# Kernel optimization log

Measured on AMD Instinct MI355X. Metric: run time of the kernel, lower is better.

The kernel has to match this reference:

```python
import jax, jax.numpy as jnp
import numpy as np

NUM_HEADS = 8
NUM_POINTS = 4


def _bilinear(img, xs, ys):
    """Bilinear sample with zero padding (grid_sample align_corners=False).
    img: [N, H, W, C]; xs, ys: [N, P] pixel-space coords. Returns [N, P, C]."""
    H, W = img.shape[1], img.shape[2]
    x0 = jnp.floor(xs)
    y0 = jnp.floor(ys)
    wx = xs - x0
    wy = ys - y0
    x0i = x0.astype(jnp.int32)
    y0i = y0.astype(jnp.int32)

    def g(ix, iy):
        valid = ((ix >= 0) & (ix < W) & (iy >= 0) & (iy < H)).astype(img.dtype)
        ixc = jnp.clip(ix, 0, W - 1)
        iyc = jnp.clip(iy, 0, H - 1)
        v = jax.vmap(lambda im, yy, xx: im[yy, xx])(img, iyc, ixc)  # [N,P,C]
        return v * valid[..., None]

    return (g(x0i, y0i) * ((1 - wx) * (1 - wy))[..., None]
            + g(x0i + 1, y0i) * (wx * (1 - wy))[..., None]
            + g(x0i, y0i + 1) * ((1 - wx) * wy)[..., None]
            + g(x0i + 1, y0i + 1) * (wx * wy)[..., None])


def setup_inputs() -> dict:
    key = jax.random.key(0)
    ks = jax.random.split(key, 10)
    BN, C, H, W = 12, 256, 40, 100
    nq = H * W
    hp = NUM_HEADS * NUM_POINTS
    s = 1.0 / np.sqrt(C).astype(np.float32)
    return {
        "img_feats": jax.random.normal(ks[0], (BN, C, H, W), jnp.float32),
        "warp_grid": jax.random.uniform(ks[1], (BN, H, W, 2), jnp.float32),
        "reference_points": jax.random.uniform(ks[2], (BN, nq, 1, 2), jnp.float32),
        "Wv": jax.random.normal(ks[3], (C, C), jnp.float32) * s,
        "bv": jnp.zeros((C,), jnp.float32),
        "Woff": jax.random.normal(ks[4], (C, hp * 2), jnp.float32) * 0.01,
        "boff": jax.random.normal(ks[5], (hp * 2,), jnp.float32) * 0.5,
        "Wattn": jax.random.normal(ks[6], (C, hp), jnp.float32) * 0.01,
        "battn": jnp.zeros((hp,), jnp.float32),
        "Wout": jax.random.normal(ks[7], (C, C), jnp.float32) * s,
        "bout": jnp.zeros((C,), jnp.float32),
    }


def reference(img_feats, warp_grid, reference_points,
              Wv, bv, Woff, boff, Wattn, battn, Wout, bout):
    BN, C, H, W = img_feats.shape
    heads, pts = NUM_HEADS, NUM_POINTS
    hd = C // heads
    nq = H * W

    feat = img_feats.transpose(0, 2, 3, 1)  # [BN, H, W, C]

    # BEVWarp: bilinear warp of image features at the projected grid ([0,1] normed)
    gx = warp_grid[..., 0].reshape(BN, -1) * W - 0.5
    gy = warp_grid[..., 1].reshape(BN, -1) * H - 0.5
    warped = _bilinear(feat, gx, gy)          # [BN, nq, C] -> value
    query = feat.reshape(BN, nq, C)           # flattened img feats -> query

    # MultiScaleDeformableAttention, num_levels=1
    v = (warped @ Wv + bv).reshape(BN, nq, heads, hd)
    off = (query @ Woff + boff).reshape(BN, nq, heads, pts, 2)
    attn = jax.nn.softmax((query @ Wattn + battn).reshape(BN, nq, heads, pts), axis=-1)

    norm = jnp.array([W, H], dtype=img_feats.dtype)
    loc = reference_points.reshape(BN, nq, 1, 1, 2) + off / norm  # [BN,nq,h,p,2]

    vh = v.transpose(0, 2, 1, 3).reshape(BN * heads, H, W, hd)
    lx = (loc[..., 0] * W - 0.5).transpose(0, 2, 1, 3).reshape(BN * heads, nq * pts)
    ly = (loc[..., 1] * H - 0.5).transpose(0, 2, 1, 3).reshape(BN * heads, nq * pts)
    sampled = _bilinear(vh, lx, ly).reshape(BN, heads, nq, pts, hd)

    agg = jnp.einsum('bhqpd,bqhp->bqhd', sampled, attn).reshape(BN, nq, C)
    out = agg @ Wout + bout + query  # output_proj + residual (dropout=0 at eval)
    return out.transpose(0, 2, 1).reshape(BN, C, H, W)
```

## Files before the change

### kernel.cpp

```cpp
#include <hip/hip_runtime.h>

#define DEVINL __device__ __forceinline__

typedef __attribute__((ext_vector_type(4))) float f32x4;
typedef __attribute__((ext_vector_type(8))) short short8;

constexpr int kBN = 12, kC = 256, kH = 40, kW = 100;
constexpr int kNQ = kH * kW;
constexpr int kM = kBN * kNQ;

DEVINL float bflo(uint p) { union { uint i; float f; } v; v.i = p << 16; return v.f; }
DEVINL float bfhi(uint p) { union { uint i; float f; } v; v.i = p & 0xffff0000u; return v.f; }
DEVINL ushort f2bf(float f) {
  union { float f; uint i; } v; v.f = f;
  uint i = v.i;
  return (ushort)((i + 0x7fffu + ((i >> 16) & 1u)) >> 16);
}
DEVINL uint pack2(float a, float b) { return (uint)f2bf(a) | ((uint)f2bf(b) << 16); }

DEVINL void mfma_bf16(f32x4& acc, short8 a, short8 b) {
  acc = __builtin_amdgcn_mfma_f32_16x16x32_bf16(a, b, acc, 0, 0, 0);
}

DEVINL void gload16(const ushort* g, char* lds) {
  __builtin_amdgcn_global_load_lds(
      (const __attribute__((address_space(1))) uint*)g,
      (__attribute__((address_space(3))) uint*)lds, 16, 0, 0);
}

DEVINL void acc8(float* acc, uint4 d, float wv) {
  acc[0] += wv * bflo(d.x); acc[1] += wv * bfhi(d.x);
  acc[2] += wv * bflo(d.y); acc[3] += wv * bfhi(d.y);
  acc[4] += wv * bflo(d.z); acc[5] += wv * bfhi(d.z);
  acc[6] += wv * bflo(d.w); acc[7] += wv * bfhi(d.w);
}

__global__ __launch_bounds__(256) void k_wt_all(const float* __restrict__ Wv,
                                                const float* __restrict__ Woff,
                                                const float* __restrict__ Wattn,
                                                const float* __restrict__ Wout,
                                                ushort* __restrict__ WvT,
                                                ushort* __restrict__ WoffT,
                                                ushort* __restrict__ WattnT,
                                                ushort* __restrict__ WoutT) {
  int idx = blockIdx.x * 256 + threadIdx.x;
  const float* W; ushort* WT; int N, base;
  if (idx < 65536)       { W = Wv;    WT = WvT;    N = 256; base = 0; }
  else if (idx < 81920)  { W = Woff;  WT = WoffT;  N = 64;  base = 65536; }
  else if (idx < 90112)  { W = Wattn; WT = WattnT; N = 32;  base = 81920; }
  else if (idx < 155648) { W = Wout;  WT = WoutT;  N = 256; base = 90112; }
  else return;
  int i = idx - base;
  int n = i >> 8, k = i & 255;
  WT[i] = f2bf(W[k * N + n]);
}

__global__ __launch_bounds__(256) void k_transpose(const float* __restrict__ img,
                                                   ushort* __restrict__ feat) {
  __shared__ ushort tile[64][66];
  int b = blockIdx.z, c0 = blockIdx.y * 64, q0 = blockIdx.x * 64;
  int t = threadIdx.x;
  int ql = t & 63, cl = t >> 6;
#pragma unroll
  for (int i = 0; i < 16; ++i) {
    int c = cl + i * 4, q = q0 + ql;
    float v = (q < kNQ) ? img[(size_t)(b * kC + c0 + c) * kNQ + q] : 0.f;
    tile[c][ql] = f2bf(v);
  }
  __syncthreads();
#pragma unroll
  for (int i = 0; i < 2; ++i) {
    int idx = t + i * 256;
    int qlo = idx >> 3, cg = idx & 7;
    int q = q0 + qlo;
    if (q < kNQ) {
      ushort tmp[8];
#pragma unroll
      for (int j = 0; j < 8; ++j) tmp[j] = tile[cg * 8 + j][qlo];
      *(uint4*)(feat + ((size_t)b * kNQ + q) * kC + c0 + cg * 8) = *(uint4*)tmp;
    }
  }
}

__global__ __launch_bounds__(256) void k_warp(const ushort* __restrict__ feat,
                                              const float* __restrict__ grid,
                                              ushort* __restrict__ warped) {
  int orig = blockIdx.x;
  int n = (orig & 7) * 750 + (orig >> 3);
  int t = threadIdx.x;
  int ql = t >> 5, g = t & 31;
  int gq = n * 8 + ql;
  int b = gq / kNQ;
  float gx = grid[(size_t)gq * 2 + 0] * kW - 0.5f;
  float gy = grid[(size_t)gq * 2 + 1] * kH - 0.5f;
  float x0f = floorf(gx), y0f = floorf(gy);
  int x0 = (int)x0f, y0 = (int)y0f;
  float wx = gx - x0f, wy = gy - y0f;
  float acc[8];
#pragma unroll
  for (int i = 0; i < 8; ++i) acc[i] = 0.f;
  const ushort* fb = feat + (size_t)b * kNQ * kC + g * 8;
#pragma unroll
  for (int ty = 0; ty < 2; ++ty) {
    int iy = y0 + ty;
    if (iy < 0 || iy >= kH) continue;
    float wyv = ty ? wy : 1.f - wy;
#pragma unroll
    for (int tx = 0; tx < 2; ++tx) {
      int ix = x0 + tx;
      if (ix < 0 || ix >= kW) continue;
      float wv = wyv * (tx ? wx : 1.f - wx);
      uint4 d = *(const uint4*)(fb + (size_t)(iy * kW + ix) * kC);
      acc8(acc, d, wv);
    }
  }
  uint o[4] = {pack2(acc[0], acc[1]), pack2(acc[2], acc[3]),
               pack2(acc[4], acc[5]), pack2(acc[6], acc[7])};
  *(uint4*)(warped + (size_t)gq * kC + g * 8) = *(uint4*)o;
}

template <int EPI>
__global__ __launch_bounds__(256) void k_gemm256(const ushort* __restrict__ A,
                                                 const ushort* __restrict__ BT,
                                                 const float* __restrict__ bias,
                                                 ushort* __restrict__ Obf,
                                                 float* __restrict__ Ofp,
                                                 const float* __restrict__ resid) {
  extern __shared__ char smem[];
  const int t = threadIdx.x, wave = t >> 6, lane = t & 63;
  const int l15 = lane & 15, l4 = lane >> 4;
  const int b = blockIdx.x / 63, mb = blockIdx.x % 63;
  const int q0 = mb * 64;
  const int nrows = (kNQ - q0 < 64) ? (kNQ - q0) : 64;
  const int n0w = wave * 64;
  const int ra = t >> 2, ca = t & 3;
  const int rac = (ra < nrows) ? ra : (nrows - 1);
  const int sca = ca ^ ((ra >> 1) & 3);
  const ushort* gA = A + ((size_t)b * kNQ + q0 + rac) * 256 + sca * 8;
  const ushort* gB = BT + (size_t)ra * 256 + sca * 8;

  f32x4 acc[4][4];
#pragma unroll
  for (int i = 0; i < 4; ++i)
#pragma unroll
    for (int j = 0; j < 4; ++j) acc[i][j] = (f32x4)0.f;

  auto STAGE = [&](int buf, int kk) {
    char* Asb = smem + buf * 20480;
    char* Bsb = Asb + 4096;
    gload16(gA + kk, Asb + t * 16);
#pragma unroll
    for (int i = 0; i < 4; ++i)
      gload16(gB + (size_t)i * 64 * 256 + kk, Bsb + (i * 256 + t) * 16);
  };

  STAGE(0, 0);
  int cur = 0;
#pragma unroll 1
  for (int step = 0; step < 8; ++step) {
    if (step < 7) {
      STAGE(cur ^ 1, (step + 1) * 32);
      asm volatile("s_waitcnt vmcnt(5)" ::: "memory");
    } else {
      asm volatile("s_waitcnt vmcnt(0)" ::: "memory");
    }
    __builtin_amdgcn_s_barrier();
    asm volatile("" ::: "memory");
    char* Asb = smem + cur * 20480;
    char* Bsb = Asb + 4096;
    short8 af[4], bf[4];
#pragma unroll
    for (int mf = 0; mf < 4; ++mf) {
      int r = mf * 16 + l15;
      int sl = l4 ^ ((r >> 1) & 3);
      af[mf] = *(const short8*)(Asb + r * 64 + sl * 16);
    }
#pragma unroll
    for (int nf = 0; nf < 4; ++nf) {
      int r = n0w + nf * 16 + l15;
      int sl = l4 ^ ((r >> 1) & 3);
      bf[nf] = *(const short8*)(Bsb + r * 64 + sl * 16);
    }
#pragma unroll
    for (int mf = 0; mf < 4; ++mf)
#pragma unroll
      for (int nf = 0; nf < 4; ++nf) mfma_bf16(acc[mf][nf], af[mf], bf[nf]);
    asm volatile("" ::: "memory");
    __builtin_amdgcn_s_barrier();
    cur ^= 1;
  }

  if (EPI == 0) {
#pragma unroll
    for (int mf = 0; mf < 4; ++mf) {
      if (mf * 16 >= nrows) continue;
      int q = q0 + mf * 16 + l4 * 4;
#pragma unroll
      for (int nf = 0; nf < 4; ++nf) {
        int col = n0w + nf * 16 + l15;
        float bv = bias[col];
        int h = col >> 5, ch = col & 31;
        ushort* dst = Obf + (size_t)(b * 8 + h) * kNQ * 32 + ch;
#pragma unroll
        for (int j = 0; j < 4; ++j)
          dst[(size_t)(q + j) * 32] = f2bf(acc[mf][nf][j] + bv);
      }
    }
  } else {
    float* Tw = (float*)(smem + wave * 4352);
#pragma unroll
    for (int nf = 0; nf < 4; ++nf) {
      float bv = bias[n0w + nf * 16 + l15];
#pragma unroll
      for (int mf = 0; mf < 4; ++mf)
#pragma unroll
        for (int j = 0; j < 4; ++j)
          Tw[l15 * 68 + mf * 16 + l4 * 4 + j] = acc[mf][nf][j] + bv;
      int c = l15, rs = l4 * 16;
      if (rs < nrows) {
        int col = n0w + nf * 16 + c;
        size_t gi = ((size_t)b * kC + col) * kNQ + q0 + rs;
#pragma unroll
        for (int k = 0; k < 4; ++k) {
          float4 tv = *(float4*)(&Tw[c * 68 + rs + k * 4]);
          float4 rv = *(const float4*)(resid + gi + k * 4);
          tv.x += rv.x; tv.y += rv.y; tv.z += rv.z; tv.w += rv.w;
          *(float4*)(Ofp + gi + k * 4) = tv;
        }
      }
    }
  }
}

__global__ __launch_bounds__(256) void k_offattn(const ushort* __restrict__ A,
                                                 const ushort* __restrict__ WoffT,
                                                 const ushort* __restrict__ WattnT,
                                                 const float* __restrict__ boff,
                                                 const float* __restrict__ battn,
                                                 const float* __restrict__ refp,
                                                 float* __restrict__ samp) {
  extern __shared__ char smem[];
  float* T = (float*)smem;
  const int t = threadIdx.x, wave = t >> 6, lane = t & 63;
  const int l15 = lane & 15, l4 = lane >> 4;
  const int b = blockIdx.x / 63, mb = blockIdx.x % 63;
  const int q0 = mb * 64;
  const int nrows = (kNQ - q0 < 64) ? (kNQ - q0) : 64;
  const int wr = wave >> 1, wc = wave & 1;
  const int ra = t >> 2, ca = t & 3;
  const int rac = (ra < nrows) ? ra : (nrows - 1);
  const int sca = ca ^ ((ra >> 1) & 3);
  const ushort* gA  = A + ((size_t)b * kNQ + q0 + rac) * 256 + sca * 8;
  const ushort* gB0 = WoffT + (size_t)ra * 256 + sca * 8;
  const ushort* gB1 = WattnT + (size_t)ra * 256 + sca * 8;

  f32x4 acc[2][3];
#pragma unroll
  for (int i = 0; i < 2; ++i)
#pragma unroll
    for (int j = 0; j < 3; ++j) acc[i][j] = (f32x4)0.f;

  auto STAGE = [&](int buf, int kk) {
    char* Asb = smem + buf * 10240;
    char* Bsb = Asb + 4096;
    gload16(gA + kk, Asb + t * 16);
    gload16(gB0 + kk, Bsb + t * 16);
    if (t < 128) gload16(gB1 + kk, Bsb + (256 + t) * 16);
  };

  STAGE(0, 0);
  int cur = 0;
#pragma unroll 1
  for (int step = 0; step < 8; ++step) {
    if (step < 7) {
      STAGE(cur ^ 1, (step + 1) * 32);
      if (wave < 2) asm volatile("s_waitcnt vmcnt(3)" ::: "memory");
      else          asm volatile("s_waitcnt vmcnt(2)" ::: "memory");
    } else {
      asm volatile("s_waitcnt vmcnt(0)" ::: "memory");
    }
    __builtin_amdgcn_s_barrier();
    asm volatile("" ::: "memory");
    char* Asb = smem + cur * 10240;
    char* Bsb = Asb + 4096;
    short8 af[2], bf[3];
#pragma unroll
    for (int mf = 0; mf < 2; ++mf) {
      int r = wr * 32 + mf * 16 + l15;
      int sl = l4 ^ ((r >> 1) & 3);
      af[mf] = *(const short8*)(Asb + r * 64 + sl * 16);
    }
#pragma unroll
    for (int nf = 0; nf < 3; ++nf) {
      int r = wc * 48 + nf * 16 + l15;
      int sl = l4 ^ ((r >> 1) & 3);
      bf[nf] = *(const short8*)(Bsb + r * 64 + sl * 16);
    }
#pragma unroll
    for (int mf = 0; mf < 2; ++mf)
#pragma unroll
      for (int nf = 0; nf < 3; ++nf) mfma_bf16(acc[mf][nf], af[mf], bf[nf]);
    asm volatile("" ::: "memory");
    __builtin_amdgcn_s_barrier();
    cur ^= 1;
  }

#pragma unroll
  for (int nf = 0; nf < 3; ++nf) {
    int col = wc * 48 + nf * 16 + l15;
    float bv = (col < 64) ? boff[col] : battn[col - 64];
#pragma unroll
    for (int mf = 0; mf < 2; ++mf)
#pragma unroll
      for (int j = 0; j < 4; ++j) {
        int row = wr * 32 + mf * 16 + l4 * 4 + j;
        T[row * 101 + col] = acc[mf][nf][j] + bv;
      }
  }
  __syncthreads();
  int row = t >> 2;
  if (row < nrows) {
    int q = q0 + row;
    float refx = refp[((size_t)b * kNQ + q) * 2 + 0] * kW - 0.5f;
    float refy = refp[((size_t)b * kNQ + q) * 2 + 1] * kH - 0.5f;
#pragma unroll
    for (int hi2 = 0; hi2 < 2; ++hi2) {
      int h = (t & 3) + hi2 * 4;
      float sx[4], sy[4], lg[4];
#pragma unroll
      for (int p = 0; p < 4; ++p) {
        sx[p] = refx + T[row * 101 + h * 8 + p * 2 + 0];
        sy[p] = refy + T[row * 101 + h * 8 + p * 2 + 1];
        lg[p] = T[row * 101 + 64 + h * 4 + p];
      }
      float mx = fmaxf(fmaxf(lg[0], lg[1]), fmaxf(lg[2], lg[3]));
      float e[4], s = 0.f;
#pragma unroll
      for (int p = 0; p < 4; ++p) { e[p] = __expf(lg[p] - mx); s += e[p]; }
      float inv = 1.f / s;
      float* dst = samp + (((size_t)(b * 8 + h) * kNQ + q) * 4) * 3;
#pragma unroll
      for (int p = 0; p < 4; ++p) {
        dst[p * 3 + 0] = sx[p];
        dst[p * 3 + 1] = sy[p];
        dst[p * 3 + 2] = e[p] * inv;
      }
    }
  }
}

__global__ __launch_bounds__(256) void k_sample(const ushort* __restrict__ v,
                                                const float* __restrict__ samp,
                                                ushort* __restrict__ agg) {
  int orig = blockIdx.x;
  int n = (orig & 7) * 756 + (orig >> 3);
  int plane = n / 63, chunk = n - plane * 63;
  int t = threadIdx.x;
  int ql = t >> 2, g = t & 3;
  int q = chunk * 64 + ql;
  if (q >= kNQ) return;
  int b = plane >> 3, h = plane & 7;
  const ushort* pv = v + (size_t)plane * kNQ * 32 + g * 8;
  const int lane = t & 63, gbase = lane & ~3;

  const float* sp = samp + (((size_t)plane * kNQ + q) * 4 + g) * 3;
  float myx = sp[0], myy = sp[1], myw = sp[2];
  float acc[8];
#pragma unroll
  for (int i = 0; i < 8; ++i) acc[i] = 0.f;
#pragma unroll
  for (int p = 0; p < 4; ++p) {
    float sxp = __shfl(myx, gbase + p);
    float syp = __shfl(myy, gbase + p);
    float wp  = __shfl(myw, gbase + p);
    float x0f = floorf(sxp), y0f = floorf(syp);
    int x0 = (int)x0f, y0 = (int)y0f;
    float wx = sxp - x0f, wy = syp - y0f;
#pragma unroll
    for (int ty = 0; ty < 2; ++ty) {
      int iy = y0 + ty;
      if (iy < 0 || iy >= kH) continue;
      float wyv = ty ? wy : 1.f - wy;
#pragma unroll
      for (int tx = 0; tx < 2; ++tx) {
        int ix = x0 + tx;
        if (ix < 0 || ix >= kW) continue;
        float wv = wp * wyv * (tx ? wx : 1.f - wx);
        uint4 d = *(const uint4*)(pv + (size_t)(iy * kW + ix) * 32);
        acc8(acc, d, wv);
      }
    }
  }
  uint o[4] = {pack2(acc[0], acc[1]), pack2(acc[2], acc[3]),
               pack2(acc[4], acc[5]), pack2(acc[6], acc[7])};
  *(uint4*)(agg + ((size_t)b * kNQ + q) * kC + h * 32 + g * 8) = *(uint4*)o;
}

extern "C" void kernel_launch(void* const* d_in, const int* in_sizes, int n_in,
                              void* d_out, int out_size, void* d_ws, size_t ws_size,
                              hipStream_t stream) {
  const float* img   = (const float*)d_in[0];
  const float* grid  = (const float*)d_in[1];
  const float* refp  = (const float*)d_in[2];
  const float* Wv    = (const float*)d_in[3];
  const float* bv    = (const float*)d_in[4];
  const float* Woff  = (const float*)d_in[5];
  const float* boff  = (const float*)d_in[6];
  const float* Wattn = (const float*)d_in[7];
  const float* battn = (const float*)d_in[8];
  const float* Wout  = (const float*)d_in[9];
  const float* bout  = (const float*)d_in[10];
  float* out = (float*)d_out;

  char* ws = (char*)d_ws;
  const size_t SZ = (size_t)kM * kC * 2;
  ushort* feat   = (ushort*)(ws);
  ushort* warped = (ushort*)(ws + SZ);
  ushort* vbuf   = (ushort*)(ws + 2 * SZ);
  float*  samp   = (float*)(ws + 3 * SZ);
  ushort* WvT    = (ushort*)(ws + 4 * SZ);
  ushort* WoffT  = (ushort*)(ws + 4 * SZ + 131072);
  ushort* WattnT = (ushort*)(ws + 4 * SZ + 131072 + 32768);
  ushort* WoutT  = (ushort*)(ws + 4 * SZ + 131072 + 32768 + 16384);
  ushort* aggb   = warped;

  k_wt_all<<<608, 256, 0, stream>>>(Wv, Woff, Wattn, Wout, WvT, WoffT, WattnT, WoutT);
  k_transpose<<<dim3(63, 4, 12), 256, 0, stream>>>(img, feat);
  k_warp<<<6000, 256, 0, stream>>>(feat, grid, warped);
  k_gemm256<0><<<756, 256, 40960, stream>>>(warped, WvT, bv, vbuf, nullptr, nullptr);
  k_offattn<<<756, 256, 25856, stream>>>(feat, WoffT, WattnT, boff, battn, refp, samp);
  k_sample<<<6048, 256, 0, stream>>>(vbuf, samp, aggb);
  k_gemm256<1><<<756, 256, 40960, stream>>>(aggb, WoutT, bout, nullptr, out, img);
}
```

Before: 122.6 us.

## Merge prep and warp/offattn kernels, retile GEMMs to 128-row blocks, read bf16 residual

Fuses the weight-transpose and image-transpose launches into one kernel, and merges the bilinear warp with the offset/attention GEMM into one launch split by block index. It also replaces the 64-row GEMM with a 128-row, 512-thread tile that covers all 256 columns, and makes the output epilogue read the residual from the bf16 transposed features instead of the fp32 image. The aim is to cut launch overhead and tail effects and to improve weight reuse per block. The costs are a residual that is now rounded to bf16, strided 2-byte residual loads, and heavier blocks that may lower occupancy.

```diff
diff --git a/kernel.cpp b/kernel.cpp
--- a/kernel.cpp
+++ b/kernel.cpp
@@ -35,222 +35,114 @@
   acc[6] += wv * bflo(d.w); acc[7] += wv * bfhi(d.w);
 }
 
-__global__ __launch_bounds__(256) void k_wt_all(const float* __restrict__ Wv,
-                                                const float* __restrict__ Woff,
-                                                const float* __restrict__ Wattn,
-                                                const float* __restrict__ Wout,
-                                                ushort* __restrict__ WvT,
-                                                ushort* __restrict__ WoffT,
-                                                ushort* __restrict__ WattnT,
-                                                ushort* __restrict__ WoutT) {
-  int idx = blockIdx.x * 256 + threadIdx.x;
-  const float* W; ushort* WT; int N, base;
-  if (idx < 65536)       { W = Wv;    WT = WvT;    N = 256; base = 0; }
-  else if (idx < 81920)  { W = Woff;  WT = WoffT;  N = 64;  base = 65536; }
-  else if (idx < 90112)  { W = Wattn; WT = WattnT; N = 32;  base = 81920; }
-  else if (idx < 155648) { W = Wout;  WT = WoutT;  N = 256; base = 90112; }
-  else return;
-  int i = idx - base;
-  int n = i >> 8, k = i & 255;
-  WT[i] = f2bf(W[k * N + n]);
-}
-
-__global__ __launch_bounds__(256) void k_transpose(const float* __restrict__ img,
-                                                   ushort* __restrict__ feat) {
+__global__ __launch_bounds__(256) void k_prep(const float* __restrict__ img,
+                                              ushort* __restrict__ feat,
+                                              const float* __restrict__ Wv,
+                                              const float* __restrict__ Woff,
+                                              const float* __restrict__ Wattn,
+                                              const float* __restrict__ Wout,
+                                              ushort* __restrict__ WvT,
+                                              ushort* __restrict__ WoffT,
+                                              ushort* __restrict__ WattnT,
+                                              ushort* __restrict__ WoutT) {
   __shared__ ushort tile[64][66];
-  int b = blockIdx.z, c0 = blockIdx.y * 64, q0 = blockIdx.x * 64;
-  int t = threadIdx.x;
-  int ql = t & 63, cl = t >> 6;
-#pragma unroll
-  for (int i = 0; i < 16; ++i) {
-    int c = cl + i * 4, q = q0 + ql;
-    float v = (q < kNQ) ? img[(size_t)(b * kC + c0 + c) * kNQ + q] : 0.f;
-    tile[c][ql] = f2bf(v);
-  }
-  __syncthreads();
-#pragma unroll
-  for (int i = 0; i < 2; ++i) {
-    int idx = t + i * 256;
-    int qlo = idx >> 3, cg = idx & 7;
-    int q = q0 + qlo;
-    if (q < kNQ) {
-      ushort tmp[8];
-#pragma unroll
-      for (int j = 0; j < 8; ++j) tmp[j] = tile[cg * 8 + j][qlo];
-      *(uint4*)(feat + ((size_t)b * kNQ + q) * kC + c0 + cg * 8) = *(uint4*)tmp;
-    }
-  }
-}
-
-__global__ __launch_bounds__(256) void k_warp(const ushort* __restrict__ feat,
-                                              const float* __restrict__ grid,
-                                              ushort* __restrict__ warped) {
-  int orig = blockIdx.x;
-  int n = (orig & 7) * 750 + (orig >> 3);
-  int t = threadIdx.x;
-  int ql = t >> 5, g = t & 31;
-  int gq = n * 8 + ql;
-  int b = gq / kNQ;
-  float gx = grid[(size_t)gq * 2 + 0] * kW - 0.5f;
-  float gy = grid[(size_t)gq * 2 + 1] * kH - 0.5f;
-  float x0f = floorf(gx), y0f = floorf(gy);
-  int x0 = (int)x0f, y0 = (int)y0f;
-  float wx = gx - x0f, wy = gy - y0f;
-  float acc[8];
-#pragma unroll
-  for (int i = 0; i < 8; ++i) acc[i] = 0.f;
-  const ushort* fb = feat + (size_t)b * kNQ * kC + g * 8;
-#pragma unroll
-  for (int ty = 0; ty < 2; ++ty) {
-    int iy = y0 + ty;
-    if (iy < 0 || iy >= kH) continue;
-    float wyv = ty ? wy : 1.f - wy;
-#pragma unroll
-    for (int tx = 0; tx < 2; ++tx) {
-      int ix = x0 + tx;
-      if (ix < 0 || ix >= kW) continue;
-      float wv = wyv * (tx ? wx : 1.f - wx);
-      uint4 d = *(const uint4*)(fb + (size_t)(iy * kW + ix) * kC);
-      acc8(acc, d, wv);
-    }
-  }
-  uint o[4] = {pack2(acc[0], acc[1]), pack2(acc[2], acc[3]),
-               pack2(acc[4], acc[5]), pack2(acc[6], acc[7])};
-  *(uint4*)(warped + (size_t)gq * kC + g * 8) = *(uint4*)o;
-}
-
-template <int EPI>
-__global__ __launch_bounds__(256) void k_gemm256(const ushort* __restrict__ A,
-                                                 const ushort* __restrict__ BT,
-                                                 const float* __restrict__ bias,
-                                                 ushort* __restrict__ Obf,
-                                                 float* __restrict__ Ofp,
-                                                 const float* __restrict__ resid) {
+  int bx = blockIdx.x, t = threadIdx.x;
+  if (bx < 3024) {
+    int qb = bx % 63, cb = (bx / 63) & 3, b = bx / 252;
+    int c0 = cb * 64, q0 = qb * 64;
+    int ql = t & 63, cl = t >> 6;
+#pragma unroll
+    for (int i = 0; i < 16; ++i) {
+      int c = cl + i * 4, q = q0 + ql;
+      float v = (q < kNQ) ? img[(size_t)(b * kC + c0 + c) * kNQ + q] : 0.f;
+      tile[c][ql] = f2bf(v);
+    }
+    __syncthreads();
+#pragma unroll
+    for (int i = 0; i < 2; ++i) {
+      int idx = t + i * 256;
+      int qlo = idx >> 3, cg = idx & 7;
+      int q = q0 + qlo;
+      if (q < kNQ) {
+        ushort tmp[8];
+#pragma unroll
+        for (int j = 0; j < 8; ++j) tmp[j] = tile[cg * 8 + j][qlo];
+        *(uint4*)(feat + ((size_t)b * kNQ + q) * kC + c0 + cg * 8) = *(uint4*)tmp;
+      }
+    }
+  } else {
+    int idx = (bx - 3024) * 256 + t;
+    const float* W; ushort* WT; int N, base;
+    if (idx < 65536)       { W = Wv;    WT = WvT;    N = 256; base = 0; }
+    else if (idx < 81920)  { W = Woff;  WT = WoffT;  N = 64;  base = 65536; }
+    else if (idx < 90112)  { W = Wattn; WT = WattnT; N = 32;  base = 81920; }
+    else if (idx < 155648) { W = Wout;  WT = WoutT;  N = 256; base = 90112; }
+    else return;
+    int i = idx - base;
+    int n = i >> 8, k = i & 255;
+    WT[i] = f2bf(W[k * N + n]);
+  }
+}
+
+__global__ __launch_bounds__(256) void k_warp_offattn(const ushort* __restrict__ feat,
+                                                      const float* __restrict__ grid,
+                                                      ushort* __restrict__ warped,
+                                                      const ushort* __restrict__ WoffT,
+                                                      const ushort* __restrict__ WattnT,
+                                                      const float* __restrict__ boff,
+                                                      const float* __restrict__ battn,
+                                                      const float* __restrict__ refp,
+                                                      float* __restrict__ samp) {
   extern __shared__ char smem[];
-  const int t = threadIdx.x, wave = t >> 6, lane = t & 63;
+  const int t = threadIdx.x;
+  int bx = blockIdx.x;
+
+  if (bx >= 756) {
+    int orig = bx - 756;
+    int n = (orig & 7) * 750 + (orig >> 3);
+    int ql = t >> 5, g = t & 31;
+    int gq = n * 8 + ql;
+    int b = gq / kNQ;
+    float gx = grid[(size_t)gq * 2 + 0] * kW - 0.5f;
+    float gy = grid[(size_t)gq * 2 + 1] * kH - 0.5f;
+    float x0f = floorf(gx), y0f = floorf(gy);
+    int x0 = (int)x0f, y0 = (int)y0f;
+    float wx = gx - x0f, wy = gy - y0f;
+    float acc[8];
+#pragma unroll
+    for (int i = 0; i < 8; ++i) acc[i] = 0.f;
+    const ushort* fb = feat + (size_t)b * kNQ * kC + g * 8;
+#pragma unroll
+    for (int ty = 0; ty < 2; ++ty) {
+      int iy = y0 + ty;
+      if (iy < 0 || iy >= kH) continue;
+      float wyv = ty ? wy : 1.f - wy;
+#pragma unroll
+      for (int tx = 0; tx < 2; ++tx) {
+        int ix = x0 + tx;
+        if (ix < 0 || ix >= kW) continue;
+        float wv = wyv * (tx ? wx : 1.f - wx);
+        uint4 d = *(const uint4*)(fb + (size_t)(iy * kW + ix) * kC);
+        acc8(acc, d, wv);
+      }
+    }
+    uint o[4] = {pack2(acc[0], acc[1]), pack2(acc[2], acc[3]),
+                 pack2(acc[4], acc[5]), pack2(acc[6], acc[7])};
+    *(uint4*)(warped + (size_t)gq * kC + g * 8) = *(uint4*)o;
+    return;
+  }
+
+  float* T = (float*)smem;
+  const int wave = t >> 6, lane = t & 63;
   const int l15 = lane & 15, l4 = lane >> 4;
-  const int b = blockIdx.x / 63, mb = blockIdx.x % 63;
-  const int q0 = mb * 64;
-  const int nrows = (kNQ - q0 < 64) ? (kNQ - q0) : 64;
-  const int n0w = wave * 64;
-  const int ra = t >> 2, ca = t & 3;
-  const int rac = (ra < nrows) ? ra : (nrows - 1);
-  const int sca = ca ^ ((ra >> 1) & 3);
-  const ushort* gA = A + ((size_t)b * kNQ + q0 + rac) * 256 + sca * 8;
-  const ushort* gB = BT + (size_t)ra * 256 + sca * 8;
-
-  f32x4 acc[4][4];
-#pragma unroll
-  for (int i = 0; i < 4; ++i)
-#pragma unroll
-    for (int j = 0; j < 4; ++j) acc[i][j] = (f32x4)0.f;
-
-  auto STAGE = [&](int buf, int kk) {
-    char* Asb = smem + buf * 20480;
-    char* Bsb = Asb + 4096;
-    gload16(gA + kk, Asb + t * 16);
-#pragma unroll
-    for (int i = 0; i < 4; ++i)
-      gload16(gB + (size_t)i * 64 * 256 + kk, Bsb + (i * 256 + t) * 16);
-  };
-
-  STAGE(0, 0);
-  int cur = 0;
-#pragma unroll 1
-  for (int step = 0; step < 8; ++step) {
-    if (step < 7) {
-      STAGE(cur ^ 1, (step + 1) * 32);
-      asm volatile("s_waitcnt vmcnt(5)" ::: "memory");
-    } else {
-      asm volatile("s_waitcnt vmcnt(0)" ::: "memory");
-    }
-    __builtin_amdgcn_s_barrier();
-    asm volatile("" ::: "memory");
-    char* Asb = smem + cur * 20480;
-    char* Bsb = Asb + 4096;
-    short8 af[4], bf[4];
-#pragma unroll
-    for (int mf = 0; mf < 4; ++mf) {
-      int r = mf * 16 + l15;
-      int sl = l4 ^ ((r >> 1) & 3);
-      af[mf] = *(const short8*)(Asb + r * 64 + sl * 16);
-    }
-#pragma unroll
-    for (int nf = 0; nf < 4; ++nf) {
-      int r = n0w + nf * 16 + l15;
-      int sl = l4 ^ ((r >> 1) & 3);
-      bf[nf] = *(const short8*)(Bsb + r * 64 + sl * 16);
-    }
-#pragma unroll
-    for (int mf = 0; mf < 4; ++mf)
-#pragma unroll
-      for (int nf = 0; nf < 4; ++nf) mfma_bf16(acc[mf][nf], af[mf], bf[nf]);
-    asm volatile("" ::: "memory");
-    __builtin_amdgcn_s_barrier();
-    cur ^= 1;
-  }
-
-  if (EPI == 0) {
-#pragma unroll
-    for (int mf = 0; mf < 4; ++mf) {
-      if (mf * 16 >= nrows) continue;
-      int q = q0 + mf * 16 + l4 * 4;
-#pragma unroll
-      for (int nf = 0; nf < 4; ++nf) {
-        int col = n0w + nf * 16 + l15;
-        float bv = bias[col];
-        int h = col >> 5, ch = col & 31;
-        ushort* dst = Obf + (size_t)(b * 8 + h) * kNQ * 32 + ch;
-#pragma unroll
-        for (int j = 0; j < 4; ++j)
-          dst[(size_t)(q + j) * 32] = f2bf(acc[mf][nf][j] + bv);
-      }
-    }
-  } else {
-    float* Tw = (float*)(smem + wave * 4352);
-#pragma unroll
-    for (int nf = 0; nf < 4; ++nf) {
-      float bv = bias[n0w + nf * 16 + l15];
-#pragma unroll
-      for (int mf = 0; mf < 4; ++mf)
-#pragma unroll
-        for (int j = 0; j < 4; ++j)
-          Tw[l15 * 68 + mf * 16 + l4 * 4 + j] = acc[mf][nf][j] + bv;
-      int c = l15, rs = l4 * 16;
-      if (rs < nrows) {
-        int col = n0w + nf * 16 + c;
-        size_t gi = ((size_t)b * kC + col) * kNQ + q0 + rs;
-#pragma unroll
-        for (int k = 0; k < 4; ++k) {
-          float4 tv = *(float4*)(&Tw[c * 68 + rs + k * 4]);
-          float4 rv = *(const float4*)(resid + gi + k * 4);
-          tv.x += rv.x; tv.y += rv.y; tv.z += rv.z; tv.w += rv.w;
-          *(float4*)(Ofp + gi + k * 4) = tv;
-        }
-      }
-    }
-  }
-}
-
-__global__ __launch_bounds__(256) void k_offattn(const ushort* __restrict__ A,
-                                                 const ushort* __restrict__ WoffT,
-                                                 const ushort* __restrict__ WattnT,
-                                                 const float* __restrict__ boff,
-                                                 const float* __restrict__ battn,
-                                                 const float* __restrict__ refp,
-                                                 float* __restrict__ samp) {
-  extern __shared__ char smem[];
-  float* T = (float*)smem;
-  const int t = threadIdx.x, wave = t >> 6, lane = t & 63;
-  const int l15 = lane & 15, l4 = lane >> 4;
-  const int b = blockIdx.x / 63, mb = blockIdx.x % 63;
+  const int b = bx / 63, mb = bx % 63;
   const int q0 = mb * 64;
   const int nrows = (kNQ - q0 < 64) ? (kNQ - q0) : 64;
   const int wr = wave >> 1, wc = wave & 1;
   const int ra = t >> 2, ca = t & 3;
   const int rac = (ra < nrows) ? ra : (nrows - 1);
   const int sca = ca ^ ((ra >> 1) & 3);
-  const ushort* gA  = A + ((size_t)b * kNQ + q0 + rac) * 256 + sca * 8;
+  const ushort* gA  = feat + ((size_t)b * kNQ + q0 + rac) * 256 + sca * 8;
   const ushort* gB0 = WoffT + (size_t)ra * 256 + sca * 8;
   const ushort* gB1 = WattnT + (size_t)ra * 256 + sca * 8;
 
@@ -344,6 +236,124 @@
         dst[p * 3 + 0] = sx[p];
         dst[p * 3 + 1] = sy[p];
         dst[p * 3 + 2] = e[p] * inv;
+      }
+    }
+  }
+}
+
+template <int EPI>
+__global__ __launch_bounds__(512) void k_gemm128(const ushort* __restrict__ A,
+                                                 const ushort* __restrict__ BT,
+                                                 const float* __restrict__ bias,
+                                                 ushort* __restrict__ Obf,
+                                                 float* __restrict__ Ofp,
+                                                 const ushort* __restrict__ feat) {
+  extern __shared__ char smem[];
+  const int t = threadIdx.x, wave = t >> 6, lane = t & 63;
+  const int l15 = lane & 15, l4 = lane >> 4;
+  const int b = blockIdx.x >> 5, mb = blockIdx.x & 31;
+  const int q0 = mb * 128;
+  const int nrows = (kNQ - q0 < 128) ? (kNQ - q0) : 128;
+  const int wr = wave >> 2, wc = wave & 3;
+  const int ra = t >> 2, ca = t & 3;
+  const int rac = (ra < nrows) ? ra : (nrows - 1);
+  const int sca = ca ^ ((ra >> 1) & 3);
+  const ushort* gA = A + ((size_t)b * kNQ + q0 + rac) * 256 + sca * 8;
+  const ushort* gB = BT + (size_t)ra * 256 + sca * 8;
+
+  f32x4 acc[4][4];
+#pragma unroll
+  for (int i = 0; i < 4; ++i)
+#pragma unroll
+    for (int j = 0; j < 4; ++j) acc[i][j] = (f32x4)0.f;
+
+  auto STAGE = [&](int buf, int kk) {
+    char* Asb = smem + buf * 24576;
+    char* Bsb = Asb + 8192;
+    gload16(gA + kk, Asb + t * 16);
+#pragma unroll
+    for (int i = 0; i < 2; ++i)
+      gload16(gB + (size_t)i * 128 * 256 + kk, Bsb + (i * 512 + t) * 16);
+  };
+
+  STAGE(0, 0);
+  int cur = 0;
+#pragma unroll 1
+  for (int step = 0; step < 8; ++step) {
+    if (step < 7) {
+      STAGE(cur ^ 1, (step + 1) * 32);
+      asm volatile("s_waitcnt vmcnt(3)" ::: "memory");
+    } else {
+      asm volatile("s_waitcnt vmcnt(0)" ::: "memory");
+    }
+    __builtin_amdgcn_s_barrier();
+    asm volatile("" ::: "memory");
+    char* Asb = smem + cur * 24576;
+    char* Bsb = Asb + 8192;
+    short8 af[4], bf[4];
+#pragma unroll
+    for (int mf = 0; mf < 4; ++mf) {
+      int r = wr * 64 + mf * 16 + l15;
+      int sl = l4 ^ ((r >> 1) & 3);
+      af[mf] = *(const short8*)(Asb + r * 64 + sl * 16);
+    }
+#pragma unroll
+    for (int nf = 0; nf < 4; ++nf) {
+      int r = wc * 64 + nf * 16 + l15;
+      int sl = l4 ^ ((r >> 1) & 3);
+      bf[nf] = *(const short8*)(Bsb + r * 64 + sl * 16);
+    }
+#pragma unroll
+    for (int mf = 0; mf < 4; ++mf)
+#pragma unroll
+      for (int nf = 0; nf < 4; ++nf) mfma_bf16(acc[mf][nf], af[mf], bf[nf]);
+    asm volatile("" ::: "memory");
+    __builtin_amdgcn_s_barrier();
+    cur ^= 1;
+  }
+
+  if (EPI == 0) {
+#pragma unroll
+    for (int mf = 0; mf < 4; ++mf) {
+      int rl = wr * 64 + mf * 16;
+      if (rl >= nrows) continue;
+      int q = q0 + rl + l4 * 4;
+#pragma unroll
+      for (int nf = 0; nf < 4; ++nf) {
+        int col = wc * 64 + nf * 16 + l15;
+        float bv = bias[col];
+        int h = col >> 5, ch = col & 31;
+        ushort* dst = Obf + (size_t)(b * 8 + h) * kNQ * 32 + ch;
+#pragma unroll
+        for (int j = 0; j < 4; ++j)
+          dst[(size_t)(q + j) * 32] = f2bf(acc[mf][nf][j] + bv);
+      }
+    }
+  } else {
+    float* Tw = (float*)(smem + wave * 4352);
+#pragma unroll
+    for (int nf = 0; nf < 4; ++nf) {
+      float bv = bias[wc * 64 + nf * 16 + l15];
+#pragma unroll
+      for (int mf = 0; mf < 4; ++mf)
+#pragma unroll
+        for (int j = 0; j < 4; ++j)
+          Tw[l15 * 68 + mf * 16 + l4 * 4 + j] = acc[mf][nf][j] + bv;
+      int c = l15, rs = l4 * 16;
+      if (wr * 64 + rs < nrows) {
+        int col = wc * 64 + nf * 16 + c;
+        size_t grow = (size_t)q0 + wr * 64 + rs;
+        size_t gi = ((size_t)b * kC + col) * kNQ + grow;
+        const ushort* fr = feat + ((size_t)b * kNQ + grow) * kC + col;
+#pragma unroll
+        for (int k = 0; k < 4; ++k) {
+          float4 tv = *(float4*)(&Tw[c * 68 + rs + k * 4]);
+          tv.x += bflo(fr[(size_t)(k * 4 + 0) * kC]);
+          tv.y += bflo(fr[(size_t)(k * 4 + 1) * kC]);
+          tv.z += bflo(fr[(size_t)(k * 4 + 2) * kC]);
+          tv.w += bflo(fr[(size_t)(k * 4 + 3) * kC]);
+          *(float4*)(Ofp + gi + k * 4) = tv;
+        }
       }
     }
   }
@@ -424,11 +434,11 @@
   ushort* WoutT  = (ushort*)(ws + 4 * SZ + 131072 + 32768 + 16384);
   ushort* aggb   = warped;
 
-  k_wt_all<<<608, 256, 0, stream>>>(Wv, Woff, Wattn, Wout, WvT, WoffT, WattnT, WoutT);
-  k_transpose<<<dim3(63, 4, 12), 256, 0, stream>>>(img, feat);
-  k_warp<<<6000, 256, 0, stream>>>(feat, grid, warped);
-  k_gemm256<0><<<756, 256, 40960, stream>>>(warped, WvT, bv, vbuf, nullptr, nullptr);
-  k_offattn<<<756, 256, 25856, stream>>>(feat, WoffT, WattnT, boff, battn, refp, samp);
+  k_prep<<<3632, 256, 0, stream>>>(img, feat, Wv, Woff, Wattn, Wout,
+                                   WvT, WoffT, WattnT, WoutT);
+  k_warp_offattn<<<6756, 256, 25856, stream>>>(feat, grid, warped, WoffT, WattnT,
+                                               boff, battn, refp, samp);
+  k_gemm128<0><<<384, 512, 49152, stream>>>(warped, WvT, bv, vbuf, nullptr, nullptr);
   k_sample<<<6048, 256, 0, stream>>>(vbuf, samp, aggb);
-  k_gemm256<1><<<756, 256, 40960, stream>>>(aggb, WoutT, bout, nullptr, out, img);
-}
+  k_gemm128<1><<<384, 512, 49152, stream>>>(aggb, WoutT, bout, nullptr, out, feat);
+}
```

Result: faster. 119.4 us (-2.6%).
